# Kernel optimization log

Hardware: AMD Instinct MI355X
Metric: run time of the kernel (lower is better)

## Reference

```python
import jax, jax.numpy as jnp
import numpy as np

N = 50000   # nodes
E = 800000  # edges (avg degree 16)
IN = 64     # in_dim
DS = 32     # in_dim // 2
HOUT = 64


def setup_inputs() -> dict:
    key = jax.random.key(0)
    ks = jax.random.split(key, 16)
    std = 0.1

    def w(k, shape):
        return std * jax.random.normal(k, shape, dtype=jnp.float32)

    z = lambda d: jnp.zeros((d,), dtype=jnp.float32)
    return {
        "x": jax.random.normal(ks[0], (N, IN), dtype=jnp.float32),
        "src": jax.random.randint(ks[1], (E,), 0, N),
        "dst": jax.random.randint(ks[2], (E,), 0, N),
        # encoders (enc_dim == in_dim branch: dim_split -> dim_split)
        "WencK": w(ks[3], (DS, DS)), "bencK": z(DS),
        "WencP1": w(ks[4], (DS, DS)), "bencP1": z(DS),
        "WencP2": w(ks[5], (DS, DS)), "bencP2": z(DS),
        # Kfun MLP: Linear(DS,HOUT) Tanh Linear(HOUT,HOUT) ReLU Linear(HOUT,HOUT)
        "WK1": w(ks[6], (DS, HOUT)), "bK1": z(HOUT),
        "WK2": w(ks[7], (HOUT, HOUT)), "bK2": z(HOUT),
        "WK3": w(ks[8], (HOUT, HOUT)), "bK3": z(HOUT),
        # Ufun MLP (same structure)
        "WU1": w(ks[9], (DS, HOUT)), "bU1": z(HOUT),
        "WU2": w(ks[10], (HOUT, HOUT)), "bU2": z(HOUT),
        "WU3": w(ks[11], (HOUT, HOUT)), "bU3": z(HOUT),
        # output heads
        "WH": w(ks[12], (HOUT, IN)), "bH": z(IN),
        "WD": w(ks[13], (IN, IN)), "bD": z(IN),
    }


def _mlp3(h, W1, b1, W2, b2, W3, b3):
    h = jnp.tanh(h @ W1 + b1)
    h = jax.nn.relu(h @ W2 + b2)
    return h @ W3 + b3


def reference(x, src, dst,
              WencK, bencK, WencP1, bencP1, WencP2, bencP2,
              WK1, bK1, WK2, bK2, WK3, bK3,
              WU1, bU1, WU2, bU2, WU3, bU3,
              WH, bH, WD, bD):
    ds = DS
    q, p = x[:, :ds], x[:, ds:]

    # getK: encode p, scatter-sum over incoming edges, node MLP
    hK = p @ WencK + bencK                              # [N, DS]
    hK_agg = jax.ops.segment_sum(hK[src], dst, num_segments=N)
    E_node = _mlp3(hK_agg, WK1, bK1, WK2, bK2, WK3, bK3)  # [N, HOUT]

    # getU: u_add_v on encoded q, edge MLP
    h1 = q @ WencP1 + bencP1
    h2 = q @ WencP2 + bencP2
    e_out = h1[src] + h2[dst]                           # [E, DS]
    E_edge = _mlp3(e_out, WU1, bU1, WU2, bU2, WU3, bU3)  # [E, HOUT]

    # getH: u_mul_e then sum into destination nodes
    E_new = jax.ops.segment_sum(E_node[src] * E_edge, dst, num_segments=N)

    # dHdx
    dH = E_new @ WH + bH                                # [N, IN]

    # get_D: dissipation term on second half of D(x), scattered over graph
    Dx = x @ WD + bD
    d_agg = jax.ops.segment_sum(Dx[:, ds:][src], dst, num_segments=N)
    d = jnp.concatenate([jnp.zeros_like(d_agg), d_agg], axis=-1)

    # dH @ J^T with J = [[0, I], [-I, 0]]  ->  [dH_p, -dH_q]
    out = jnp.concatenate([dH[:, ds:], -dH[:, :ds]], axis=-1) - d
    return out
```

## Files before the change

### kernel.cpp

```cpp
#include <hip/hip_runtime.h>
#include <hip/hip_bf16.h>

#define NN 50000
#define EE 800000
#define IN_DIM 64
#define DS_DIM 32
#define HOUT_DIM 64

#define K4_WAVES 10000
#define K4_EPW   80
#define K4_C     5
#define K4_NWG   (K4_WAVES / 4)

#define XA_EPW 64
#define XA_NWG 3125

#define HIST_BLOCKS 3125
#define ENC_BLOCKS  6250

#define SCAN_NB 196

#define XPS 72

typedef __attribute__((ext_vector_type(8))) short bf16x8;
typedef __attribute__((ext_vector_type(4))) float f32x4;

__device__ __forceinline__ float fast_tanh(float x) {
    float e = __builtin_amdgcn_exp2f(x * 2.885390082f);
    return 1.f - 2.f * __builtin_amdgcn_rcpf(e + 1.f);
}

__device__ __forceinline__ void atomAddF(float* p, float v) {
#if defined(__AMDGCN__)
    unsafeAtomicAdd(p, v);
#else
    atomicAdd(p, v);
#endif
}

__device__ __forceinline__ short f2b(float f) {
    union { __hip_bfloat16 h; short s; } u;
    u.h = __float2bfloat16(f);
    return u.s;
}
__device__ __forceinline__ float b2f(unsigned short u) {
    return __uint_as_float(((unsigned int)u) << 16);
}

__device__ __forceinline__ int xcd_swz(int bid, int nwg) {
    int xcd = bid & 7, idx = bid >> 3;
    int q = nwg >> 3, r = nwg & 7;
    return (xcd < r ? xcd * (q + 1) : r * (q + 1) + (xcd - r) * q) + idx;
}

__global__ void kmega0(const int* __restrict__ dst, int* __restrict__ cnt,
                       const float* __restrict__ x,
                       const float* __restrict__ WencP1, const float* __restrict__ bencP1,
                       const float* __restrict__ WencP2, const float* __restrict__ bencP2,
                       __hip_bfloat16* __restrict__ h1b, __hip_bfloat16* __restrict__ h2b,
                       __hip_bfloat16* __restrict__ xb) {
    if (blockIdx.x < HIST_BLOCKS) {
        int e = blockIdx.x * 256 + threadIdx.x;
        atomicAdd(&cnt[dst[e]], 1);
    } else {
        int tid = (blockIdx.x - HIST_BLOCKS) * 256 + threadIdx.x;
        int n = tid >> 5;
        int j = tid & 31;
        if (n >= NN) return;
        const float* xr = x + (size_t)n * IN_DIM;
        float a1 = bencP1[j], a2 = bencP2[j];
        #pragma unroll
        for (int k = 0; k < 32; k++) {
            float q = xr[k];
            a1 = fmaf(q, WencP1[k * 32 + j], a1);
            a2 = fmaf(q, WencP2[k * 32 + j], a2);
        }
        union { __hip_bfloat16 h; short s; } u1, u2, u3, u4;
        u1.s = f2b(a1); u2.s = f2b(a2);
        h1b[(size_t)n * 32 + j] = u1.h;
        h2b[(size_t)n * 32 + j] = u2.h;
        u3.s = f2b(xr[j]); u4.s = f2b(xr[32 + j]);
        xb[(size_t)n * 64 + j] = u3.h;
        xb[(size_t)n * 64 + 32 + j] = u4.h;
    }
}

__global__ void kscanA(const int* __restrict__ cnt, int* __restrict__ blocksum) {
    __shared__ int s[256];
    int t = threadIdx.x;
    int i = blockIdx.x * 256 + t;
    s[t] = (i < NN) ? cnt[i] : 0;
    __syncthreads();
    #pragma unroll
    for (int off = 128; off > 0; off >>= 1) {
        if (t < off) s[t] += s[t + off];
        __syncthreads();
    }
    if (t == 0) blocksum[blockIdx.x] = s[0];
}

__global__ void kscanB(const int* __restrict__ blocksum, int* __restrict__ blockoff) {
    __shared__ int part[256];
    int t = threadIdx.x;
    int v = (t < SCAN_NB) ? blocksum[t] : 0;
    part[t] = v;
    __syncthreads();
    for (int off = 1; off < 256; off <<= 1) {
        int u = (t >= off) ? part[t - off] : 0;
        __syncthreads();
        part[t] += u;
        __syncthreads();
    }
    if (t < SCAN_NB) blockoff[t] = part[t] - v;
}

__global__ void kscanC(const int* __restrict__ cnt, const int* __restrict__ blockoff,
                       int* __restrict__ rowptr) {
    __shared__ int part[256];
    int t = threadIdx.x;
    int i = blockIdx.x * 256 + t;
    int v = (i < NN) ? cnt[i] : 0;
    part[t] = v;
    __syncthreads();
    for (int off = 1; off < 256; off <<= 1) {
        int u = (t >= off) ? part[t - off] : 0;
        __syncthreads();
        part[t] += u;
        __syncthreads();
    }
    if (i < NN) {
        int incl = blockoff[blockIdx.x] + part[t];
        rowptr[i] = incl - v;
        if (i == NN - 1) rowptr[NN] = incl;
    }
}

__global__ void kscatter(const int* __restrict__ src, const int* __restrict__ dst,
                         const int* __restrict__ rowptr, int* __restrict__ fill,
                         int2* __restrict__ epack) {
    int e = blockIdx.x * 256 + threadIdx.x;
    if (e >= EE) return;
    int d = dst[e];
    int pos = rowptr[d] + atomicAdd(&fill[d], 1);
    int2 p; p.x = src[e]; p.y = d;
    epack[pos] = p;
}

__global__ void __launch_bounds__(256) kxagg3(const int2* __restrict__ epack,
                                              const __hip_bfloat16* __restrict__ xb,
                                              float* __restrict__ xagg) {
    int sbid = xcd_swz(blockIdx.x, XA_NWG);
    int w = sbid * 4 + (threadIdx.x >> 6);
    int lane = threadIdx.x & 63;
    int base = w * XA_EPW;
    const unsigned short* xu = reinterpret_cast<const unsigned short*>(xb);

    int2 myep = epack[base + lane];
    int sarr = myep.x, darr = myep.y;

    float v0 = b2f(xu[(size_t)__shfl(sarr, 0) * 64 + lane]);
    float v1 = b2f(xu[(size_t)__shfl(sarr, 1) * 64 + lane]);
    float v2 = b2f(xu[(size_t)__shfl(sarr, 2) * 64 + lane]);
    float v3 = b2f(xu[(size_t)__shfl(sarr, 3) * 64 + lane]);
    int cd = __shfl(darr, 0);
    float carry = 0.f;

#define XA_STEP(vv, T)                                                        \
    {                                                                         \
        float cur = vv;                                                       \
        if ((T) + 4 < XA_EPW)                                                 \
            vv = b2f(xu[(size_t)__shfl(sarr, (T) + 4) * 64 + lane]);          \
        int d = __shfl(darr, (T));                                            \
        if (d != cd) {                                                        \
            atomAddF(&xagg[(size_t)cd * 64 + lane], carry);                   \
            cd = d; carry = 0.f;                                              \
        }                                                                     \
        carry += cur;                                                         \
    }

    for (int tb = 0; tb < XA_EPW; tb += 4) {
        XA_STEP(v0, tb);
        XA_STEP(v1, tb + 1);
        XA_STEP(v2, tb + 2);
        XA_STEP(v3, tb + 3);
    }
#undef XA_STEP
    atomAddF(&xagg[(size_t)cd * 64 + lane], carry);
}

__global__ void __launch_bounds__(256) k3ab(
    const float* __restrict__ xagg, const int* __restrict__ cnt,
    const float* __restrict__ WencK, const float* __restrict__ bencK,
    const float* __restrict__ WD, const float* __restrict__ bD,
    const float* __restrict__ WK1, const float* __restrict__ bK1,
    const float* __restrict__ WK2, const float* __restrict__ bK2,
    const float* __restrict__ WK3, const float* __restrict__ bK3,
    float* __restrict__ dagg, __hip_bfloat16* __restrict__ EnodeB)
{
    __shared__ unsigned short xpose[4][16 * XPS];
    const int wid  = threadIdx.x >> 6;
    const int lane = threadIdx.x & 63;
    const int g = lane >> 4;
    const int r = lane & 15;
    unsigned short* xp = xpose[wid];

    bf16x8 bwd[2][2];
    #pragma unroll
    for (int c = 0; c < 2; c++)
        #pragma unroll
        for (int nd = 0; nd < 2; nd++)
            #pragma unroll
            for (int i = 0; i < 8; i++)
                bwd[c][nd][i] = f2b(WD[(c * 32 + g * 8 + i) * 64 + 32 + nd * 16 + r]);
    bf16x8 bwk[2];
    #pragma unroll
    for (int nd = 0; nd < 2; nd++)
        #pragma unroll
        for (int i = 0; i < 8; i++)
            bwk[nd][i] = f2b(WencK[(g * 8 + i) * 32 + nd * 16 + r]);
    bf16x8 b1[4];
    #pragma unroll
    for (int nt = 0; nt < 4; nt++)
        #pragma unroll
        for (int i = 0; i < 8; i++)
            b1[nt][i] = f2b(WK1[(g * 8 + i) * 64 + nt * 16 + r]);
    bf16x8 b2[2][4], b3[2][4];
    #pragma unroll
    for (int c = 0; c < 2; c++)
        #pragma unroll
        for (int nt = 0; nt < 4; nt++)
            #pragma unroll
            for (int i = 0; i < 8; i++) {
                b2[c][nt][i] = f2b(WK2[(c * 32 + g * 8 + i) * 64 + nt * 16 + r]);
                b3[c][nt][i] = f2b(WK3[(c * 32 + g * 8 + i) * 64 + nt * 16 + r]);
            }
    float bdv[2], bkv[2];
    #pragma unroll
    for (int nd = 0; nd < 2; nd++) {
        bdv[nd] = bD[32 + nd * 16 + r];
        bkv[nd] = bencK[nd * 16 + r];
    }
    float bias1[4], bias2[4], bias3[4];
    #pragma unroll
    for (int nt = 0; nt < 4; nt++) {
        bias1[nt] = bK1[nt * 16 + r];
        bias2[nt] = bK2[nt * 16 + r];
        bias3[nt] = bK3[nt * 16 + r];
    }

    const int ntiles = NN / 16;
    const int wave = blockIdx.x * 4 + wid;
    const int nw = gridDim.x * 4;
    const f32x4 zero = {0.f, 0.f, 0.f, 0.f};

    for (int tile = wave; tile < ntiles; tile += nw) {
        bf16x8 ax0, ax1;
        {
            const float* xr = xagg + ((size_t)tile * 16 + r) * 64 + g * 8;
            float4 p0 = *reinterpret_cast<const float4*>(xr);
            float4 p1 = *reinterpret_cast<const float4*>(xr + 4);
            float4 p2 = *reinterpret_cast<const float4*>(xr + 32);
            float4 p3 = *reinterpret_cast<const float4*>(xr + 36);
            ax0[0] = f2b(p0.x); ax0[1] = f2b(p0.y); ax0[2] = f2b(p0.z); ax0[3] = f2b(p0.w);
            ax0[4] = f2b(p1.x); ax0[5] = f2b(p1.y); ax0[6] = f2b(p1.z); ax0[7] = f2b(p1.w);
            ax1[0] = f2b(p2.x); ax1[1] = f2b(p2.y); ax1[2] = f2b(p2.z); ax1[3] = f2b(p2.w);
            ax1[4] = f2b(p3.x); ax1[5] = f2b(p3.y); ax1[6] = f2b(p3.z); ax1[7] = f2b(p3.w);
        }
        float cq[4];
        #pragma unroll
        for (int q = 0; q < 4; q++) cq[q] = (float)cnt[tile * 16 + g * 4 + q];

        f32x4 accd[2];
        #pragma unroll
        for (int nd = 0; nd < 2; nd++) {
            accd[nd] = __builtin_amdgcn_mfma_f32_16x16x32_bf16(ax0, bwd[0][nd], zero, 0, 0, 0);
            accd[nd] = __builtin_amdgcn_mfma_f32_16x16x32_bf16(ax1, bwd[1][nd], accd[nd], 0, 0, 0);
        }
        #pragma unroll
        for (int nd = 0; nd < 2; nd++)
            #pragma unroll
            for (int q = 0; q < 4; q++)
                dagg[((size_t)tile * 16 + g * 4 + q) * 32 + nd * 16 + r] =
                    accd[nd][q] + cq[q] * bdv[nd];

        f32x4 acch[2];
        #pragma unroll
        for (int nd = 0; nd < 2; nd++)
            acch[nd] = __builtin_amdgcn_mfma_f32_16x16x32_bf16(ax1, bwk[nd], zero, 0, 0, 0);
        #pragma unroll
        for (int nd = 0; nd < 2; nd++)
            #pragma unroll
            for (int q = 0; q < 4; q++)
                xp[(g * 4 + q) * XPS + nd * 16 + r] = (unsigned short)f2b(acch[nd][q] + cq[q] * bkv[nd]);

        bf16x8 af = *reinterpret_cast<const bf16x8*>(xp + r * XPS + g * 8);
        f32x4 acc[4];
        #pragma unroll
        for (int nt = 0; nt < 4; nt++)
            acc[nt] = __builtin_amdgcn_mfma_f32_16x16x32_bf16(af, b1[nt], zero, 0, 0, 0);
        #pragma unroll
        for (int nt = 0; nt < 4; nt++)
            #pragma unroll
            for (int q = 0; q < 4; q++)
                xp[(g * 4 + q) * XPS + nt * 16 + r] = (unsigned short)f2b(fast_tanh(acc[nt][q] + bias1[nt]));

        f32x4 acc2[4] = {zero, zero, zero, zero};
        #pragma unroll
        for (int c = 0; c < 2; c++) {
            bf16x8 a2 = *reinterpret_cast<const bf16x8*>(xp + r * XPS + c * 32 + g * 8);
            #pragma unroll
            for (int nt = 0; nt < 4; nt++)
                acc2[nt] = __builtin_amdgcn_mfma_f32_16x16x32_bf16(a2, b2[c][nt], acc2[nt], 0, 0, 0);
        }
        #pragma unroll
        for (int nt = 0; nt < 4; nt++)
            #pragma unroll
            for (int q = 0; q < 4; q++)
                xp[(g * 4 + q) * XPS + nt * 16 + r] = (unsigned short)f2b(fmaxf(acc2[nt][q] + bias2[nt], 0.f));

        f32x4 acc3[4] = {zero, zero, zero, zero};
        #pragma unroll
        for (int c = 0; c < 2; c++) {
            bf16x8 a3 = *reinterpret_cast<const bf16x8*>(xp + r * XPS + c * 32 + g * 8);
            #pragma unroll
            for (int nt = 0; nt < 4; nt++)
                acc3[nt] = __builtin_amdgcn_mfma_f32_16x16x32_bf16(a3, b3[c][nt], acc3[nt], 0, 0, 0);
        }
        #pragma unroll
        for (int nt = 0; nt < 4; nt++)
            #pragma unroll
            for (int q = 0; q < 4; q++)
                xp[(g * 4 + q) * XPS + nt * 16 + r] = (unsigned short)f2b(acc3[nt][q] + bias3[nt]);
        {
            uint4 w0 = *reinterpret_cast<const uint4*>(xp + r * XPS + g * 16);
            uint4 w1 = *reinterpret_cast<const uint4*>(xp + r * XPS + g * 16 + 8);
            unsigned int* ob = reinterpret_cast<unsigned int*>(EnodeB + ((size_t)tile * 16 + r) * 64 + g * 16);
            *reinterpret_cast<uint4*>(ob) = w0;
            *reinterpret_cast<uint4*>(ob + 4) = w1;
        }
    }
}

__global__ void __launch_bounds__(256) k4_mfma(
    const int2* __restrict__ epack,
    const __hip_bfloat16* __restrict__ h1b, const __hip_bfloat16* __restrict__ h2b,
    const __hip_bfloat16* __restrict__ EnodeB, float* __restrict__ Enew,
    const float* __restrict__ WU1, const float* __restrict__ bU1,
    const float* __restrict__ WU2, const float* __restrict__ bU2,
    const float* __restrict__ WU3, const float* __restrict__ bU3)
{
    __shared__ unsigned short xpose[4][16 * XPS];
    const int wid  = threadIdx.x >> 6;
    const int lane = threadIdx.x & 63;
    const int g = lane >> 4;
    const int r = lane & 15;
    unsigned short* xp = xpose[wid];

    bf16x8 b1[4];
    #pragma unroll
    for (int nt = 0; nt < 4; nt++) {
        #pragma unroll
        for (int i = 0; i < 8; i++)
            b1[nt][i] = f2b(WU1[(g * 8 + i) * 64 + nt * 16 + r]);
    }
    bf16x8 b2[2][4], b3[2][4];
    #pragma unroll
    for (int c = 0; c < 2; c++) {
        #pragma unroll
        for (int nt = 0; nt < 4; nt++) {
            #pragma unroll
            for (int i = 0; i < 8; i++) {
                b2[c][nt][i] = f2b(WU2[(c * 32 + g * 8 + i) * 64 + nt * 16 + r]);
                b3[c][nt][i] = f2b(WU3[(c * 32 + g * 8 + i) * 64 + nt * 16 + r]);
            }
        }
    }
    float bias1[4], bias2[4], bias3[4];
    #pragma unroll
    for (int nt = 0; nt < 4; nt++) {
        bias1[nt] = bU1[nt * 16 + r];
        bias2[nt] = bU2[nt * 16 + r];
        bias3[nt] = bU3[nt * 16 + r];
    }

    const int sbid = xcd_swz(blockIdx.x, K4_NWG);
    const int wave = sbid * 4 + wid;
    const int base = wave * K4_EPW;
    const f32x4 zero = {0.f, 0.f, 0.f, 0.f};
    const unsigned short* enB = reinterpret_cast<const unsigned short*>(EnodeB);

    int   cd[4] = {-1, -1, -1, -1};
    float cv0[4] = {0, 0, 0, 0}, cv1[4] = {0, 0, 0, 0},
          cv2[4] = {0, 0, 0, 0}, cv3[4] = {0, 0, 0, 0};

    int2 ep = epack[base + r * K4_C];
    uint4 v1 = *reinterpret_cast<const uint4*>(h1b + (size_t)ep.x * 32 + g * 8);
    uint4 v2 = *reinterpret_cast<const uint4*>(h2b + (size_t)ep.y * 32 + g * 8);

    for (int t = 0; t < K4_C; t++) {
        const int s_me = ep.x, d_me = ep.y;
        union { uint4 v; unsigned int u[4]; } u1, u2;
        u1.v = v1; u2.v = v2;
        if (t + 1 < K4_C) {
            ep = epack[base + r * K4_C + t + 1];
            v1 = *reinterpret_cast<const uint4*>(h1b + (size_t)ep.x * 32 + g * 8);
            v2 = *reinterpret_cast<const uint4*>(h2b + (size_t)ep.y * 32 + g * 8);
        }

        int dq[4];
        float en0[4], en1[4], en2[4], en3[4];
        #pragma unroll
        for (int q = 0; q < 4; q++) {
            const int er = g * 4 + q;
            const int ssv = __shfl(s_me, er);
            dq[q] = __shfl(d_me, er);
            const unsigned short* enp = enB + (size_t)ssv * 64 + r;
            en0[q] = b2f(enp[0]);
            en1[q] = b2f(enp[16]);
            en2[q] = b2f(enp[32]);
            en3[q] = b2f(enp[48]);
        }

        bf16x8 a;
        #pragma unroll
        for (int w = 0; w < 4; w++) {
            float lo = b2f((unsigned short)(u1.u[w] & 0xffff)) + b2f((unsigned short)(u2.u[w] & 0xffff));
            float hi = b2f((unsigned short)(u1.u[w] >> 16))    + b2f((unsigned short)(u2.u[w] >> 16));
            a[2 * w]     = f2b(lo);
            a[2 * w + 1] = f2b(hi);
        }
        __builtin_amdgcn_s_setprio(1);
        f32x4 acc[4];
        #pragma unroll
        for (int nt = 0; nt < 4; nt++)
            acc[nt] = __builtin_amdgcn_mfma_f32_16x16x32_bf16(a, b1[nt], zero, 0, 0, 0);

        #pragma unroll
        for (int nt = 0; nt < 4; nt++) {
            #pragma unroll
            for (int q = 0; q < 4; q++)
                xp[(g * 4 + q) * XPS + nt * 16 + r] = (unsigned short)f2b(fast_tanh(acc[nt][q] + bias1[nt]));
        }

        f32x4 acc2[4] = {zero, zero, zero, zero};
        #pragma unroll
        for (int c = 0; c < 2; c++) {
            bf16x8 af = *reinterpret_cast<const bf16x8*>(xp + r * XPS + c * 32 + g * 8);
            #pragma unroll
            for (int nt = 0; nt < 4; nt++)
                acc2[nt] = __builtin_amdgcn_mfma_f32_16x16x32_bf16(af, b2[c][nt], acc2[nt], 0, 0, 0);
        }
        #pragma unroll
        for (int nt = 0; nt < 4; nt++) {
            #pragma unroll
            for (int q = 0; q < 4; q++)
                xp[(g * 4 + q) * XPS + nt * 16 + r] = (unsigned short)f2b(fmaxf(acc2[nt][q] + bias2[nt], 0.f));
        }

        f32x4 acc3[4] = {zero, zero, zero, zero};
        #pragma unroll
        for (int c = 0; c < 2; c++) {
            bf16x8 af = *reinterpret_cast<const bf16x8*>(xp + r * XPS + c * 32 + g * 8);
            #pragma unroll
            for (int nt = 0; nt < 4; nt++)
                acc3[nt] = __builtin_amdgcn_mfma_f32_16x16x32_bf16(af, b3[c][nt], acc3[nt], 0, 0, 0);
        }
        __builtin_amdgcn_s_setprio(0);

        #pragma unroll
        for (int q = 0; q < 4; q++) {
            float w0 = (acc3[0][q] + bias3[0]) * en0[q];
            float w1 = (acc3[1][q] + bias3[1]) * en1[q];
            float w2 = (acc3[2][q] + bias3[2]) * en2[q];
            float w3 = (acc3[3][q] + bias3[3]) * en3[q];
            if (dq[q] == cd[q]) {
                cv0[q] += w0; cv1[q] += w1; cv2[q] += w2; cv3[q] += w3;
            } else {
                if (cd[q] >= 0) {
                    float* ew = Enew + (size_t)cd[q] * 64 + r;
                    atomAddF(ew,      cv0[q]);
                    atomAddF(ew + 16, cv1[q]);
                    atomAddF(ew + 32, cv2[q]);
                    atomAddF(ew + 48, cv3[q]);
                }
                cd[q] = dq[q];
                cv0[q] = w0; cv1[q] = w1; cv2[q] = w2; cv3[q] = w3;
            }
        }
    }
    #pragma unroll
    for (int q = 0; q < 4; q++) {
        if (cd[q] >= 0) {
            float* ew = Enew + (size_t)cd[q] * 64 + r;
            atomAddF(ew,      cv0[q]);
            atomAddF(ew + 16, cv1[q]);
            atomAddF(ew + 32, cv2[q]);
            atomAddF(ew + 48, cv3[q]);
        }
    }
}

__global__ void k5_out(const float* __restrict__ Enew, const float* __restrict__ dagg,
                       const float* __restrict__ WH, const float* __restrict__ bH,
                       float* __restrict__ out) {
    int tid = blockIdx.x * blockDim.x + threadIdx.x;
    int n = tid >> 6;
    int j = tid & 63;
    if (n >= NN) return;
    const float* er = Enew + (size_t)n * 64;
    int jj = (j < 32) ? (j + 32) : (j - 32);
    float acc = bH[jj];
    #pragma unroll
    for (int k = 0; k < 64; k++) acc = fmaf(er[k], WH[k * 64 + jj], acc);
    float val;
    if (j < 32) val = acc;
    else        val = -acc - dagg[(size_t)n * 32 + (j - 32)];
    out[tid] = val;
}

extern "C" void kernel_launch(void* const* d_in, const int* in_sizes, int n_in,
                              void* d_out, int out_size, void* d_ws, size_t ws_size,
                              hipStream_t stream) {
    const float* x      = (const float*)d_in[0];
    const int*   src    = (const int*)d_in[1];
    const int*   dst    = (const int*)d_in[2];
    const float* WencK  = (const float*)d_in[3];
    const float* bencK  = (const float*)d_in[4];
    const float* WencP1 = (const float*)d_in[5];
    const float* bencP1 = (const float*)d_in[6];
    const float* WencP2 = (const float*)d_in[7];
    const float* bencP2 = (const float*)d_in[8];
    const float* WK1    = (const float*)d_in[9];
    const float* bK1    = (const float*)d_in[10];
    const float* WK2    = (const float*)d_in[11];
    const float* bK2    = (const float*)d_in[12];
    const float* WK3    = (const float*)d_in[13];
    const float* bK3    = (const float*)d_in[14];
    const float* WU1    = (const float*)d_in[15];
    const float* bU1    = (const float*)d_in[16];
    const float* WU2    = (const float*)d_in[17];
    const float* bU2    = (const float*)d_in[18];
    const float* WU3    = (const float*)d_in[19];
    const float* bU3    = (const float*)d_in[20];
    const float* WH     = (const float*)d_in[21];
    const float* bH     = (const float*)d_in[22];
    const float* WD     = (const float*)d_in[23];
    const float* bD     = (const float*)d_in[24];
    float* out = (float*)d_out;

    float* xagg = (float*)d_ws;
    float* Enew = xagg + (size_t)NN * 64;
    float* dagg = Enew + (size_t)NN * 64;
    __hip_bfloat16* h1b    = (__hip_bfloat16*)(dagg + (size_t)NN * 32);
    __hip_bfloat16* h2b    = h1b + (size_t)NN * 32;
    __hip_bfloat16* EnodeB = h2b + (size_t)NN * 32;
    __hip_bfloat16* xb     = EnodeB + (size_t)NN * 64;
    int*  cnt      = (int*)(xb + (size_t)NN * 64);
    int*  fill     = cnt + NN;
    int*  rowptr   = fill + NN;
    int*  blocksum = rowptr + NN + 2;
    int*  blockoff = blocksum + 256;
    int2* epack    = (int2*)(blockoff + 256);
    size_t need = (size_t)NN * 160 * 4 + (size_t)NN * 192 * 2
                + ((size_t)NN * 3 + 2 + 512) * 4 + (size_t)EE * 8;
    if (ws_size < need) return;

    hipMemsetAsync(cnt, 0, (size_t)2 * NN * sizeof(int), stream);
    hipMemsetAsync(xagg, 0, (size_t)NN * 128 * sizeof(float), stream);

    kmega0<<<HIST_BLOCKS + ENC_BLOCKS, 256, 0, stream>>>(
        dst, cnt, x, WencP1, bencP1, WencP2, bencP2, h1b, h2b, xb);
    kscanA<<<SCAN_NB, 256, 0, stream>>>(cnt, blocksum);
    kscanB<<<1, 256, 0, stream>>>(blocksum, blockoff);
    kscanC<<<SCAN_NB, 256, 0, stream>>>(cnt, blockoff, rowptr);
    kscatter<<<HIST_BLOCKS, 256, 0, stream>>>(src, dst, rowptr, fill, epack);
    kxagg3<<<XA_NWG, 256, 0, stream>>>(epack, xb, xagg);
    k3ab<<<782, 256, 0, stream>>>(xagg, cnt, WencK, bencK, WD, bD,
                                  WK1, bK1, WK2, bK2, WK3, bK3, dagg, EnodeB);
    k4_mfma<<<K4_NWG, 256, 0, stream>>>(epack, h1b, h2b, EnodeB, Enew,
                                        WU1, bU1, WU2, bU2, WU3, bU3);
    k5_out<<<(NN * 64 + 255) / 256, 256, 0, stream>>>(Enew, dagg, WH, bH, out);
}
```

Baseline: 289.4 us.

## Split packed edge array into SoA src/dst and fold h1+h2 add into MFMA

Replaces the interleaved int2 edge array with separate src and dst index arrays, filling dst from rowptr in a new kdfill kernel so the scatter only writes 4-byte src values. In the edge MLP, the per-element bf16 h1+h2 sum is dropped; the first layer instead accumulates two MFMAs, one per operand, which avoids a bf16 round of the sum and the unpack/convert ALU work. This adds one kernel launch and doubles the first-layer MFMA count, and the consuming kernels now issue two index loads instead of one.

```diff
diff --git a/kernel.cpp b/kernel.cpp
--- a/kernel.cpp
+++ b/kernel.cpp
@@ -135,18 +135,27 @@
     }
 }
 
+__global__ void __launch_bounds__(256) kdfill(const int* __restrict__ rowptr,
+                                              int* __restrict__ dstp) {
+    int w = (blockIdx.x * blockDim.x + threadIdx.x) >> 6;
+    int lane = threadIdx.x & 63;
+    if (w >= NN) return;
+    int lo = rowptr[w], hi = rowptr[w + 1];
+    for (int p = lo + lane; p < hi; p += 64) dstp[p] = w;
+}
+
 __global__ void kscatter(const int* __restrict__ src, const int* __restrict__ dst,
                          const int* __restrict__ rowptr, int* __restrict__ fill,
-                         int2* __restrict__ epack) {
+                         int* __restrict__ srcp) {
     int e = blockIdx.x * 256 + threadIdx.x;
     if (e >= EE) return;
     int d = dst[e];
     int pos = rowptr[d] + atomicAdd(&fill[d], 1);
-    int2 p; p.x = src[e]; p.y = d;
-    epack[pos] = p;
-}
-
-__global__ void __launch_bounds__(256) kxagg3(const int2* __restrict__ epack,
+    srcp[pos] = src[e];
+}
+
+__global__ void __launch_bounds__(256) kxagg3(const int* __restrict__ srcp,
+                                              const int* __restrict__ dstp,
                                               const __hip_bfloat16* __restrict__ xb,
                                               float* __restrict__ xagg) {
     int sbid = xcd_swz(blockIdx.x, XA_NWG);
@@ -155,8 +164,8 @@
     int base = w * XA_EPW;
     const unsigned short* xu = reinterpret_cast<const unsigned short*>(xb);
 
-    int2 myep = epack[base + lane];
-    int sarr = myep.x, darr = myep.y;
+    int sarr = srcp[base + lane];
+    int darr = dstp[base + lane];
 
     float v0 = b2f(xu[(size_t)__shfl(sarr, 0) * 64 + lane]);
     float v1 = b2f(xu[(size_t)__shfl(sarr, 1) * 64 + lane]);
@@ -342,7 +351,7 @@
 }
 
 __global__ void __launch_bounds__(256) k4_mfma(
-    const int2* __restrict__ epack,
+    const int* __restrict__ srcp, const int* __restrict__ dstp,
     const __hip_bfloat16* __restrict__ h1b, const __hip_bfloat16* __restrict__ h2b,
     const __hip_bfloat16* __restrict__ EnodeB, float* __restrict__ Enew,
     const float* __restrict__ WU1, const float* __restrict__ bU1,
@@ -393,18 +402,20 @@
     float cv0[4] = {0, 0, 0, 0}, cv1[4] = {0, 0, 0, 0},
           cv2[4] = {0, 0, 0, 0}, cv3[4] = {0, 0, 0, 0};
 
-    int2 ep = epack[base + r * K4_C];
-    uint4 v1 = *reinterpret_cast<const uint4*>(h1b + (size_t)ep.x * 32 + g * 8);
-    uint4 v2 = *reinterpret_cast<const uint4*>(h2b + (size_t)ep.y * 32 + g * 8);
+    int sp = srcp[base + r * K4_C];
+    int dp = dstp[base + r * K4_C];
+    uint4 v1 = *reinterpret_cast<const uint4*>(h1b + (size_t)sp * 32 + g * 8);
+    uint4 v2 = *reinterpret_cast<const uint4*>(h2b + (size_t)dp * 32 + g * 8);
 
     for (int t = 0; t < K4_C; t++) {
-        const int s_me = ep.x, d_me = ep.y;
-        union { uint4 v; unsigned int u[4]; } u1, u2;
-        u1.v = v1; u2.v = v2;
+        const int s_me = sp, d_me = dp;
+        union { uint4 v; bf16x8 b; } ua1, ua2;
+        ua1.v = v1; ua2.v = v2;
         if (t + 1 < K4_C) {
-            ep = epack[base + r * K4_C + t + 1];
-            v1 = *reinterpret_cast<const uint4*>(h1b + (size_t)ep.x * 32 + g * 8);
-            v2 = *reinterpret_cast<const uint4*>(h2b + (size_t)ep.y * 32 + g * 8);
+            sp = srcp[base + r * K4_C + t + 1];
+            dp = dstp[base + r * K4_C + t + 1];
+            v1 = *reinterpret_cast<const uint4*>(h1b + (size_t)sp * 32 + g * 8);
+            v2 = *reinterpret_cast<const uint4*>(h2b + (size_t)dp * 32 + g * 8);
         }
 
         int dq[4];
@@ -421,19 +432,13 @@
             en3[q] = b2f(enp[48]);
         }
 
-        bf16x8 a;
-        #pragma unroll
-        for (int w = 0; w < 4; w++) {
-            float lo = b2f((unsigned short)(u1.u[w] & 0xffff)) + b2f((unsigned short)(u2.u[w] & 0xffff));
-            float hi = b2f((unsigned short)(u1.u[w] >> 16))    + b2f((unsigned short)(u2.u[w] >> 16));
-            a[2 * w]     = f2b(lo);
-            a[2 * w + 1] = f2b(hi);
-        }
         __builtin_amdgcn_s_setprio(1);
         f32x4 acc[4];
         #pragma unroll
-        for (int nt = 0; nt < 4; nt++)
-            acc[nt] = __builtin_amdgcn_mfma_f32_16x16x32_bf16(a, b1[nt], zero, 0, 0, 0);
+        for (int nt = 0; nt < 4; nt++) {
+            acc[nt] = __builtin_amdgcn_mfma_f32_16x16x32_bf16(ua2.b, b1[nt], zero, 0, 0, 0);
+            acc[nt] = __builtin_amdgcn_mfma_f32_16x16x32_bf16(ua1.b, b1[nt], acc[nt], 0, 0, 0);
+        }
 
         #pragma unroll
         for (int nt = 0; nt < 4; nt++) {
@@ -560,7 +565,8 @@
     int*  rowptr   = fill + NN;
     int*  blocksum = rowptr + NN + 2;
     int*  blockoff = blocksum + 256;
-    int2* epack    = (int2*)(blockoff + 256);
+    int*  srcp     = blockoff + 256;
+    int*  dstp     = srcp + EE;
     size_t need = (size_t)NN * 160 * 4 + (size_t)NN * 192 * 2
                 + ((size_t)NN * 3 + 2 + 512) * 4 + (size_t)EE * 8;
     if (ws_size < need) return;
@@ -573,11 +579,12 @@
     kscanA<<<SCAN_NB, 256, 0, stream>>>(cnt, blocksum);
     kscanB<<<1, 256, 0, stream>>>(blocksum, blockoff);
     kscanC<<<SCAN_NB, 256, 0, stream>>>(cnt, blockoff, rowptr);
-    kscatter<<<HIST_BLOCKS, 256, 0, stream>>>(src, dst, rowptr, fill, epack);
-    kxagg3<<<XA_NWG, 256, 0, stream>>>(epack, xb, xagg);
+    kdfill<<<(NN * 64 + 255) / 256, 256, 0, stream>>>(rowptr, dstp);
+    kscatter<<<HIST_BLOCKS, 256, 0, stream>>>(src, dst, rowptr, fill, srcp);
+    kxagg3<<<XA_NWG, 256, 0, stream>>>(srcp, dstp, xb, xagg);
     k3ab<<<782, 256, 0, stream>>>(xagg, cnt, WencK, bencK, WD, bD,
                                   WK1, bK1, WK2, bK2, WK3, bK3, dagg, EnodeB);
-    k4_mfma<<<K4_NWG, 256, 0, stream>>>(epack, h1b, h2b, EnodeB, Enew,
+    k4_mfma<<<K4_NWG, 256, 0, stream>>>(srcp, dstp, h1b, h2b, EnodeB, Enew,
                                         WU1, bU1, WU2, bU2, WU3, bU3);
     k5_out<<<(NN * 64 + 255) / 256, 256, 0, stream>>>(Enew, dagg, WH, bH, out);
 }
```

Result: no change. 294.9 us (+1.9%).
